# Performance work log

Measured on AMD Instinct MI355X. Metric: run time of the kernel, lower is better.

Reference implementation:

```python
import jax, jax.numpy as jnp
import numpy as np

MARGIN = 1.0
EPS = 1e-6  # torch F.pairwise_distance default eps, added elementwise to (x - y)
NEG_INF = -1e30
POS_INF = 1e30


def _pairwise_dist_matrix(e):
    # D[i,j] = || e_i - e_j + EPS ||_2, expanded so we never materialize [B,B,D]:
    # ||d + eps||^2 = ||d||^2 + 2*eps*sum(d) + Dfeat*eps^2,  d = e_i - e_j
    sq = jnp.sum(e * e, axis=1)          # [B]
    s = jnp.sum(e, axis=1)               # [B]
    d2 = (sq[:, None] + sq[None, :] - 2.0 * (e @ e.T)
          + 2.0 * EPS * (s[:, None] - s[None, :])
          + e.shape[1] * (EPS * EPS))
    return jnp.sqrt(jnp.maximum(d2, 0.0))  # [B,B]


def _pdist(x, y):
    # F.pairwise_distance(p=2): ||x - y + eps||
    return jnp.sqrt(jnp.sum(jnp.square(x - y + EPS), axis=-1))


def setup_inputs() -> dict:
    B, D = 4096, 128
    key = jax.random.key(0)
    k1, k2, k3, k4 = jax.random.split(key, 4)
    embedding = jax.random.normal(k1, (B, D), dtype=jnp.float32)
    # label space == batch, each label appears exactly once in the batch
    target_idx = jax.random.permutation(k2, B).astype(jnp.int32)
    positive_idxs = jax.random.bernoulli(k3, 0.02, (B, B))  # [B, L] label-space mask
    negative_idxs = jax.random.bernoulli(k4, 0.5, (B, B))
    return {"embedding": embedding, "target_idx": target_idx,
            "positive_idxs": positive_idxs, "negative_idxs": negative_idxs}


def reference(embedding, target_idx, positive_idxs, negative_idxs):
    # Mining happens under no_grad in the original module.
    dm = jax.lax.stop_gradient(_pairwise_dist_matrix(embedding))  # [B,B]
    # batch j is a positive/negative candidate for anchor i iff its label is flagged
    pos_mask = positive_idxs[:, target_idx]  # [B,B] bool
    neg_mask = negative_idxs[:, target_idx]
    pos_idx = jnp.argmax(jnp.where(pos_mask, dm, NEG_INF), axis=1)  # hardest positive
    neg_idx = jnp.argmin(jnp.where(neg_mask, dm, POS_INF), axis=1)  # hardest negative
    valid = jnp.any(pos_mask, axis=1) & jnp.any(neg_mask, axis=1)
    a = embedding
    p = embedding[pos_idx]
    n = embedding[neg_idx]
    ap = _pdist(a, p)
    an = _pdist(a, n)
    pn = _pdist(p, n)
    loss = jax.nn.relu(ap - jnp.minimum(an, pn) + MARGIN)
    w = valid.astype(loss.dtype)
    return jnp.sum(loss * w) / jnp.maximum(jnp.sum(w), 1.0)
```

## Files before the change

kernel.cpp:

```cpp
#include <hip/hip_runtime.h>
#include <stdint.h>

#define BN 4096
#define DD 128
#define EPSF 1e-6f
#define MARGINF 1.0f

typedef unsigned long long ull;
typedef unsigned short ushort;
typedef short short8 __attribute__((ext_vector_type(8)));
typedef float f32x4 __attribute__((ext_vector_type(4)));

__device__ __forceinline__ unsigned int ord_f32(float f) {
    unsigned int u = __float_as_uint(f);
    return (u & 0x80000000u) ? ~u : (u | 0x80000000u);
}
__device__ __forceinline__ ushort bf16_rne(float x) {
    unsigned int u = __float_as_uint(x);
    return (ushort)((u + 0x7FFFu + ((u >> 16) & 1u)) >> 16);
}
__device__ __forceinline__ unsigned int pack8(ull v) {
    v &= 0x0F0F0F0F0F0F0F0FULL;
    v = (v | (v >> 4)) & 0x00FF00FF00FF00FFULL;
    v = (v | (v >> 8)) & 0x0000FFFF0000FFFFULL;
    v = (v | (v >> 16));
    return (unsigned int)v;
}

__global__ void k_prep(const float* __restrict__ e, const int* __restrict__ tidx,
                       float* __restrict__ sq, float* __restrict__ s,
                       int* __restrict__ inv, ull* __restrict__ pk, ull* __restrict__ nk,
                       unsigned int* __restrict__ ehi) {
    int w = threadIdx.x >> 6, lane = threadIdx.x & 63;
    int row = blockIdx.x * 4 + w;
    float2 v = ((const float2*)(e + (size_t)row * DD))[lane];
    ushort hx = bf16_rne(v.x), hy = bf16_rne(v.y);
    ehi[row * 64 + lane] = (unsigned int)hx | ((unsigned int)hy << 16);
    float ss = v.x + v.y;
    float qq = v.x * v.x + v.y * v.y;
    #pragma unroll
    for (int off = 32; off > 0; off >>= 1) {
        ss += __shfl_down(ss, off);
        qq += __shfl_down(qq, off);
    }
    if (lane == 0) {
        sq[row] = qq; s[row] = ss;
        inv[tidx[row]] = row;
        pk[row] = 0ULL; nk[row] = 0ULL;
    }
}

__global__ __launch_bounds__(256, 4)
void k_select(const ushort* __restrict__ ehi,
              const int* __restrict__ pos, const int* __restrict__ neg,
              const float* __restrict__ sq, const float* __restrict__ s,
              const int* __restrict__ inv,
              ull* __restrict__ pkey, ull* __restrict__ nkey) {
    __shared__ __align__(16) char smem[36864];
    __shared__ float rjl[128];
    __shared__ int jvs[128];

    const int tid = threadIdx.x;
    const int lane = tid & 63;
    const int w = tid >> 6, wr = w >> 1, wc = w & 1;
    const int lrow = lane & 15, quad = lane >> 4;
    const int i0 = blockIdx.x * 128, c0 = blockIdx.y * 128;

    if (tid < 128) {
        int j = inv[c0 + tid];
        jvs[tid] = j;
        rjl[tid] = sq[j] - 2.0f * EPSF * s[j];
    }

    unsigned char* nibP = (unsigned char*)smem;
    unsigned char* nibN = (unsigned char*)(smem + 4096);
    {
        const int4* pbase = (const int4*)(pos + (size_t)i0 * BN + c0);
        const int4* nbase = (const int4*)(neg + (size_t)i0 * BN + c0);
        #pragma unroll
        for (int p = 0; p < 16; p++) {
            int flat = p * 256 + tid;
            int r = flat >> 5, q = flat & 31;
            size_t idx = (size_t)r * (BN / 4) + q;
            int4 P = pbase[idx];
            int4 N = nbase[idx];
            unsigned int pm = (unsigned int)(P.x != 0) | ((unsigned int)(P.y != 0) << 1)
                            | ((unsigned int)(P.z != 0) << 2) | ((unsigned int)(P.w != 0) << 3);
            unsigned int nm = (unsigned int)(N.x != 0) | ((unsigned int)(N.y != 0) << 1)
                            | ((unsigned int)(N.z != 0) << 2) | ((unsigned int)(N.w != 0) << 3);
            nibP[r * 32 + q] = (unsigned char)pm;
            nibN[r * 32 + q] = (unsigned char)nm;
        }
    }
    __syncthreads();

    ull pw, nw;
    {
        int off = (tid >> 1) * 32 + (tid & 1) * 16;
        ull lo = *(const ull*)(nibP + off);
        ull hi = *(const ull*)(nibP + off + 8);
        pw = (ull)pack8(lo) | ((ull)pack8(hi) << 32);
        lo = *(const ull*)(nibN + off);
        hi = *(const ull*)(nibN + off + 8);
        nw = (ull)pack8(lo) | ((ull)pack8(hi) << 32);
    }
    __syncthreads();

    ushort* Bst = (ushort*)smem;
    #pragma unroll
    for (int it = 0; it < 8; it++) {
        int slot = it * 256 + tid;
        int r = slot >> 4, seg16 = slot & 15;
        int kc = seg16 >> 3, seg = seg16 & 7;
        int jr = jvs[r];
        int4 v = ((const int4*)ehi)[(size_t)jr * 16 + seg16];
        *(int4*)(Bst + (kc * 128 + r) * 72 + seg * 8) = v;
    }
    __syncthreads();

    f32x4 acc[4][4];
    #pragma unroll
    for (int rt = 0; rt < 4; rt++)
        #pragma unroll
        for (int ct = 0; ct < 4; ct++)
            acc[rt][ct] = (f32x4){0.f, 0.f, 0.f, 0.f};

    size_t abase[4];
    #pragma unroll
    for (int rt = 0; rt < 4; rt++)
        abase[rt] = (size_t)(i0 + wr * 64 + rt * 16 + lrow) * DD + quad * 8;

    #pragma unroll
    for (int ks = 0; ks < 4; ks++) {
        const int kc = ks >> 1, ksl = ks & 1;
        short8 ah[4];
        #pragma unroll
        for (int rt = 0; rt < 4; rt++)
            ah[rt] = *(const short8*)(ehi + abase[rt] + ks * 32);
        #pragma unroll
        for (int ct = 0; ct < 4; ct++) {
            const int bo = (kc * 128 + wc * 64 + ct * 16 + lrow) * 72 + ksl * 32 + quad * 8;
            short8 bh = *(const short8*)(Bst + bo);
            #pragma unroll
            for (int rt = 0; rt < 4; rt++)
                acc[rt][ct] = __builtin_amdgcn_mfma_f32_16x16x32_bf16(ah[rt], bh, acc[rt][ct], 0, 0, 0);
        }
    }

    __syncthreads();
    ull* pbl = (ull*)smem;
    ull* nbl = (ull*)(smem + 2048);
    pbl[tid] = pw;
    nbl[tid] = nw;
    __syncthreads();

    int jcol[4]; float rjc[4];
    #pragma unroll
    for (int ct = 0; ct < 4; ct++) {
        jcol[ct] = jvs[wc * 64 + ct * 16 + lrow];
        rjc[ct] = rjl[wc * 64 + ct * 16 + lrow];
    }
    ull* scrp = (ull*)(smem + 4096);
    ull* scrn = (ull*)(smem + 20480);
    #pragma unroll
    for (int rt = 0; rt < 4; rt++)
        #pragma unroll
        for (int t = 0; t < 4; t++) {
            const int row = wr * 64 + rt * 16 + quad * 4 + t;
            ull pb = pbl[row * 2 + wc] >> lrow;
            ull nb = nbl[row * 2 + wc] >> lrow;
            float bpv = -3.4e38f, bnv = 3.4e38f;
            int bpi = 0x7FFFFFFF, bni = 0x7FFFFFFF;
            #pragma unroll
            for (int ct = 0; ct < 4; ct++) {
                float m = rjc[ct] - 2.0f * acc[rt][ct][t];
                int j = jcol[ct];
                if ((pb >> (ct * 16)) & 1ULL) {
                    if (m > bpv || (m == bpv && j < bpi)) { bpv = m; bpi = j; }
                }
                if ((nb >> (ct * 16)) & 1ULL) {
                    if (m < bnv || (m == bnv && j < bni)) { bnv = m; bni = j; }
                }
            }
            ull kp = (bpi == 0x7FFFFFFF) ? 0ULL
                   : (((ull)ord_f32(bpv) << 32) | (ull)(0xFFFFFFFFu - (unsigned)bpi));
            ull kn = (bni == 0x7FFFFFFF) ? 0ULL
                   : (((ull)(~ord_f32(bnv)) << 32) | (ull)(0xFFFFFFFFu - (unsigned)bni));
            ull op = __shfl_xor(kp, 8); if (op > kp) kp = op;
            ull on = __shfl_xor(kn, 8); if (on > kn) kn = on;
            if (lrow < 8) {
                scrp[(wc * 8 + lrow) * 128 + row] = kp;
                scrn[(wc * 8 + lrow) * 128 + row] = kn;
            }
        }
    __syncthreads();
    if (tid < 128) {
        ull kp = 0ULL, kn = 0ULL;
        #pragma unroll
        for (int k = 0; k < 16; k++) {
            ull v = scrp[k * 128 + tid]; if (v > kp) kp = v;
            v = scrn[k * 128 + tid];     if (v > kn) kn = v;
        }
        if (kp) atomicMax(&pkey[i0 + tid], kp);
        if (kn) atomicMax(&nkey[i0 + tid], kn);
    }
}

__global__ void k_loss(const float* __restrict__ e,
                       const ull* __restrict__ pkey, const ull* __restrict__ nkey,
                       float* __restrict__ partials) {
    int w = threadIdx.x >> 6, lane = threadIdx.x & 63;
    int row = blockIdx.x * 4 + w;
    ull pk = pkey[row], nk = nkey[row];
    float loss = 0.0f, wt = 0.0f;
    if (pk != 0ULL && nk != 0ULL) {
        int pi = (int)(0xFFFFFFFFu - (unsigned)(pk & 0xFFFFFFFFu));
        int ni = (int)(0xFFFFFFFFu - (unsigned)(nk & 0xFFFFFFFFu));
        float2 av = ((const float2*)(e + (size_t)row * DD))[lane];
        float2 pv = ((const float2*)(e + (size_t)pi * DD))[lane];
        float2 nv = ((const float2*)(e + (size_t)ni * DD))[lane];
        float dx, dy;
        dx = av.x - pv.x + EPSF; dy = av.y - pv.y + EPSF;
        float ap2 = dx * dx + dy * dy;
        dx = av.x - nv.x + EPSF; dy = av.y - nv.y + EPSF;
        float an2 = dx * dx + dy * dy;
        dx = pv.x - nv.x + EPSF; dy = pv.y - nv.y + EPSF;
        float pn2 = dx * dx + dy * dy;
        #pragma unroll
        for (int off = 32; off > 0; off >>= 1) {
            ap2 += __shfl_down(ap2, off);
            an2 += __shfl_down(an2, off);
            pn2 += __shfl_down(pn2, off);
        }
        if (lane == 0) {
            float ap = sqrtf(ap2), an = sqrtf(an2), pn = sqrtf(pn2);
            loss = fmaxf(ap - fminf(an, pn) + MARGINF, 0.0f);
            wt = 1.0f;
        }
    }
    __shared__ float sl[4], sw[4];
    if (lane == 0) { sl[w] = loss; sw[w] = wt; }
    __syncthreads();
    if (threadIdx.x == 0) {
        partials[blockIdx.x * 2 + 0] = sl[0] + sl[1] + sl[2] + sl[3];
        partials[blockIdx.x * 2 + 1] = sw[0] + sw[1] + sw[2] + sw[3];
    }
}

__global__ void k_final(const float* __restrict__ partials, float* __restrict__ out) {
    int tid = threadIdx.x;
    float L = 0.0f, W = 0.0f;
    for (int i = 0; i < 4; i++) {
        int idx = tid + i * 256;
        L += partials[idx * 2];
        W += partials[idx * 2 + 1];
    }
    #pragma unroll
    for (int off = 32; off > 0; off >>= 1) {
        L += __shfl_down(L, off);
        W += __shfl_down(W, off);
    }
    __shared__ float sl[4], sw[4];
    int w = tid >> 6, lane = tid & 63;
    if (lane == 0) { sl[w] = L; sw[w] = W; }
    __syncthreads();
    if (tid == 0) {
        float Lt = sl[0] + sl[1] + sl[2] + sl[3];
        float Wt = sw[0] + sw[1] + sw[2] + sw[3];
        out[0] = Lt / fmaxf(Wt, 1.0f);
    }
}

extern "C" void kernel_launch(void* const* d_in, const int* in_sizes, int n_in,
                              void* d_out, int out_size, void* d_ws, size_t ws_size,
                              hipStream_t stream) {
    const float* e    = (const float*)d_in[0];
    const int*   tidx = (const int*)d_in[1];
    const int*   pos  = (const int*)d_in[2];
    const int*   neg  = (const int*)d_in[3];
    float* out = (float*)d_out;

    ull* pkey  = (ull*)d_ws;
    ull* nkey  = pkey + BN;
    float* sq  = (float*)(nkey + BN);
    float* s   = sq + BN;
    int* inv   = (int*)(s + BN);
    float* partials = (float*)(inv + BN);
    unsigned int* ehi = (unsigned int*)(partials + 2048);

    k_prep<<<BN / 4, 256, 0, stream>>>(e, tidx, sq, s, inv, pkey, nkey, ehi);
    dim3 grid(BN / 128, BN / 128);
    k_select<<<grid, 256, 0, stream>>>((const ushort*)ehi, pos, neg,
                                       sq, s, inv, pkey, nkey);
    k_loss<<<BN / 4, 256, 0, stream>>>(e, pkey, nkey, partials);
    k_final<<<1, 256, 0, stream>>>(partials, out);
}
```

Before: 185.9 us.

## Read masks directly in epilogue, pad scratch, fuse final reduction into loss kernel

The mask tiles are no longer staged in shared memory as nibble bitmasks. Each lane now reads its pos/neg int32 mask elements straight from global memory in the MFMA epilogue, and the argmax/argmin is simplified to a single combined-key max. The scratch reduction layout is padded (stride 17) to avoid LDS bank conflicts, and the final-sum kernel is merged into k_loss with a last-block-done atomic counter, which saves one launch. The epilogue mask loads are strided (16 lanes contiguous per row), so coalescing is worse than the old int4 bulk loads and the kernel may stall on the MFMA tail.

```diff
diff --git a/kernel.cpp b/kernel.cpp
--- a/kernel.cpp
+++ b/kernel.cpp
@@ -19,20 +19,14 @@
     unsigned int u = __float_as_uint(x);
     return (ushort)((u + 0x7FFFu + ((u >> 16) & 1u)) >> 16);
 }
-__device__ __forceinline__ unsigned int pack8(ull v) {
-    v &= 0x0F0F0F0F0F0F0F0FULL;
-    v = (v | (v >> 4)) & 0x00FF00FF00FF00FFULL;
-    v = (v | (v >> 8)) & 0x0000FFFF0000FFFFULL;
-    v = (v | (v >> 16));
-    return (unsigned int)v;
-}
 
 __global__ void k_prep(const float* __restrict__ e, const int* __restrict__ tidx,
                        float* __restrict__ sq, float* __restrict__ s,
                        int* __restrict__ inv, ull* __restrict__ pk, ull* __restrict__ nk,
-                       unsigned int* __restrict__ ehi) {
+                       unsigned int* __restrict__ ehi, unsigned int* __restrict__ cnt) {
     int w = threadIdx.x >> 6, lane = threadIdx.x & 63;
     int row = blockIdx.x * 4 + w;
+    if (blockIdx.x == 0 && threadIdx.x == 0) cnt[0] = 0u;
     float2 v = ((const float2*)(e + (size_t)row * DD))[lane];
     ushort hx = bf16_rne(v.x), hy = bf16_rne(v.y);
     ehi[row * 64 + lane] = (unsigned int)hx | ((unsigned int)hy << 16);
@@ -71,39 +65,6 @@
         jvs[tid] = j;
         rjl[tid] = sq[j] - 2.0f * EPSF * s[j];
     }
-
-    unsigned char* nibP = (unsigned char*)smem;
-    unsigned char* nibN = (unsigned char*)(smem + 4096);
-    {
-        const int4* pbase = (const int4*)(pos + (size_t)i0 * BN + c0);
-        const int4* nbase = (const int4*)(neg + (size_t)i0 * BN + c0);
-        #pragma unroll
-        for (int p = 0; p < 16; p++) {
-            int flat = p * 256 + tid;
-            int r = flat >> 5, q = flat & 31;
-            size_t idx = (size_t)r * (BN / 4) + q;
-            int4 P = pbase[idx];
-            int4 N = nbase[idx];
-            unsigned int pm = (unsigned int)(P.x != 0) | ((unsigned int)(P.y != 0) << 1)
-                            | ((unsigned int)(P.z != 0) << 2) | ((unsigned int)(P.w != 0) << 3);
-            unsigned int nm = (unsigned int)(N.x != 0) | ((unsigned int)(N.y != 0) << 1)
-                            | ((unsigned int)(N.z != 0) << 2) | ((unsigned int)(N.w != 0) << 3);
-            nibP[r * 32 + q] = (unsigned char)pm;
-            nibN[r * 32 + q] = (unsigned char)nm;
-        }
-    }
-    __syncthreads();
-
-    ull pw, nw;
-    {
-        int off = (tid >> 1) * 32 + (tid & 1) * 16;
-        ull lo = *(const ull*)(nibP + off);
-        ull hi = *(const ull*)(nibP + off + 8);
-        pw = (ull)pack8(lo) | ((ull)pack8(hi) << 32);
-        lo = *(const ull*)(nibN + off);
-        hi = *(const ull*)(nibN + off + 8);
-        nw = (ull)pack8(lo) | ((ull)pack8(hi) << 32);
-    }
     __syncthreads();
 
     ushort* Bst = (ushort*)smem;
@@ -148,58 +109,58 @@
     }
 
     __syncthreads();
-    ull* pbl = (ull*)smem;
-    ull* nbl = (ull*)(smem + 2048);
-    pbl[tid] = pw;
-    nbl[tid] = nw;
-    __syncthreads();
-
-    int jcol[4]; float rjc[4];
+
+    ull* scrp = (ull*)smem;
+    ull* scrn = (ull*)(smem + 17408);
+
+    unsigned int jninv[4]; float rjc[4];
     #pragma unroll
     for (int ct = 0; ct < 4; ct++) {
-        jcol[ct] = jvs[wc * 64 + ct * 16 + lrow];
-        rjc[ct] = rjl[wc * 64 + ct * 16 + lrow];
-    }
-    ull* scrp = (ull*)(smem + 4096);
-    ull* scrn = (ull*)(smem + 20480);
-    #pragma unroll
-    for (int rt = 0; rt < 4; rt++)
+        int cc = wc * 64 + ct * 16 + lrow;
+        jninv[ct] = 0xFFFFFFFFu - (unsigned int)jvs[cc];
+        rjc[ct] = rjl[cc];
+    }
+
+    const size_t mrow0 = (size_t)(i0 + wr * 64 + quad * 4) * BN + (size_t)(c0 + wc * 64 + lrow);
+    const int rbase = wr * 64 + quad * 4;
+
+    #pragma unroll
+    for (int rt = 0; rt < 4; rt++) {
         #pragma unroll
         for (int t = 0; t < 4; t++) {
-            const int row = wr * 64 + rt * 16 + quad * 4 + t;
-            ull pb = pbl[row * 2 + wc] >> lrow;
-            ull nb = nbl[row * 2 + wc] >> lrow;
-            float bpv = -3.4e38f, bnv = 3.4e38f;
-            int bpi = 0x7FFFFFFF, bni = 0x7FFFFFFF;
+            const size_t mb = mrow0 + (size_t)(rt * 16 + t) * BN;
+            int pd[4], nd[4];
+            #pragma unroll
+            for (int ct = 0; ct < 4; ct++) {
+                pd[ct] = pos[mb + ct * 16];
+                nd[ct] = neg[mb + ct * 16];
+            }
+            ull kp = 0ULL, kn = 0ULL;
             #pragma unroll
             for (int ct = 0; ct < 4; ct++) {
                 float m = rjc[ct] - 2.0f * acc[rt][ct][t];
-                int j = jcol[ct];
-                if ((pb >> (ct * 16)) & 1ULL) {
-                    if (m > bpv || (m == bpv && j < bpi)) { bpv = m; bpi = j; }
-                }
-                if ((nb >> (ct * 16)) & 1ULL) {
-                    if (m < bnv || (m == bnv && j < bni)) { bnv = m; bni = j; }
-                }
+                unsigned int om = ord_f32(m);
+                ull keyp = ((ull)om << 32) | (ull)jninv[ct];
+                ull keyn = ((ull)(om ^ 0xFFFFFFFFu) << 32) | (ull)jninv[ct];
+                if (pd[ct] != 0 && keyp > kp) kp = keyp;
+                if (nd[ct] != 0 && keyn > kn) kn = keyn;
             }
-            ull kp = (bpi == 0x7FFFFFFF) ? 0ULL
-                   : (((ull)ord_f32(bpv) << 32) | (ull)(0xFFFFFFFFu - (unsigned)bpi));
-            ull kn = (bni == 0x7FFFFFFF) ? 0ULL
-                   : (((ull)(~ord_f32(bnv)) << 32) | (ull)(0xFFFFFFFFu - (unsigned)bni));
             ull op = __shfl_xor(kp, 8); if (op > kp) kp = op;
             ull on = __shfl_xor(kn, 8); if (on > kn) kn = on;
             if (lrow < 8) {
-                scrp[(wc * 8 + lrow) * 128 + row] = kp;
-                scrn[(wc * 8 + lrow) * 128 + row] = kn;
+                const int row = rbase + rt * 16 + t;
+                scrp[row * 17 + wc * 8 + lrow] = kp;
+                scrn[row * 17 + wc * 8 + lrow] = kn;
             }
         }
+    }
     __syncthreads();
     if (tid < 128) {
         ull kp = 0ULL, kn = 0ULL;
         #pragma unroll
         for (int k = 0; k < 16; k++) {
-            ull v = scrp[k * 128 + tid]; if (v > kp) kp = v;
-            v = scrn[k * 128 + tid];     if (v > kn) kn = v;
+            ull v = scrp[tid * 17 + k]; if (v > kp) kp = v;
+            v = scrn[tid * 17 + k];     if (v > kn) kn = v;
         }
         if (kp) atomicMax(&pkey[i0 + tid], kp);
         if (kn) atomicMax(&nkey[i0 + tid], kn);
@@ -208,7 +169,8 @@
 
 __global__ void k_loss(const float* __restrict__ e,
                        const ull* __restrict__ pkey, const ull* __restrict__ nkey,
-                       float* __restrict__ partials) {
+                       float* __restrict__ partials, unsigned int* __restrict__ cnt,
+                       float* __restrict__ out) {
     int w = threadIdx.x >> 6, lane = threadIdx.x & 63;
     int row = blockIdx.x * 4 + w;
     ull pk = pkey[row], nk = nkey[row];
@@ -239,35 +201,42 @@
         }
     }
     __shared__ float sl[4], sw[4];
+    __shared__ unsigned int rank;
     if (lane == 0) { sl[w] = loss; sw[w] = wt; }
     __syncthreads();
     if (threadIdx.x == 0) {
-        partials[blockIdx.x * 2 + 0] = sl[0] + sl[1] + sl[2] + sl[3];
-        partials[blockIdx.x * 2 + 1] = sw[0] + sw[1] + sw[2] + sw[3];
-    }
-}
-
-__global__ void k_final(const float* __restrict__ partials, float* __restrict__ out) {
-    int tid = threadIdx.x;
-    float L = 0.0f, W = 0.0f;
-    for (int i = 0; i < 4; i++) {
-        int idx = tid + i * 256;
-        L += partials[idx * 2];
-        W += partials[idx * 2 + 1];
-    }
-    #pragma unroll
-    for (int off = 32; off > 0; off >>= 1) {
-        L += __shfl_down(L, off);
-        W += __shfl_down(W, off);
-    }
-    __shared__ float sl[4], sw[4];
-    int w = tid >> 6, lane = tid & 63;
-    if (lane == 0) { sl[w] = L; sw[w] = W; }
-    __syncthreads();
-    if (tid == 0) {
-        float Lt = sl[0] + sl[1] + sl[2] + sl[3];
-        float Wt = sw[0] + sw[1] + sw[2] + sw[3];
-        out[0] = Lt / fmaxf(Wt, 1.0f);
+        float L = sl[0] + sl[1] + sl[2] + sl[3];
+        float W = sw[0] + sw[1] + sw[2] + sw[3];
+        __hip_atomic_store(&partials[blockIdx.x * 2 + 0], L, __ATOMIC_RELAXED, __HIP_MEMORY_SCOPE_AGENT);
+        __hip_atomic_store(&partials[blockIdx.x * 2 + 1], W, __ATOMIC_RELAXED, __HIP_MEMORY_SCOPE_AGENT);
+        __threadfence();
+        rank = atomicAdd(cnt, 1u);
+    }
+    __syncthreads();
+    if (rank == (unsigned)(gridDim.x - 1)) {
+        __threadfence();
+        int tid = threadIdx.x;
+        float L = 0.0f, W = 0.0f;
+        #pragma unroll
+        for (int i = 0; i < 4; i++) {
+            int idx = tid + i * 256;
+            L += __hip_atomic_load(&partials[idx * 2 + 0], __ATOMIC_RELAXED, __HIP_MEMORY_SCOPE_AGENT);
+            W += __hip_atomic_load(&partials[idx * 2 + 1], __ATOMIC_RELAXED, __HIP_MEMORY_SCOPE_AGENT);
+        }
+        #pragma unroll
+        for (int off = 32; off > 0; off >>= 1) {
+            L += __shfl_down(L, off);
+            W += __shfl_down(W, off);
+        }
+        __shared__ float fl[4], fw[4];
+        int w2 = tid >> 6, l2 = tid & 63;
+        if (l2 == 0) { fl[w2] = L; fw[w2] = W; }
+        __syncthreads();
+        if (tid == 0) {
+            float Lt = fl[0] + fl[1] + fl[2] + fl[3];
+            float Wt = fw[0] + fw[1] + fw[2] + fw[3];
+            out[0] = Lt / fmaxf(Wt, 1.0f);
+        }
     }
 }
 
@@ -287,11 +256,11 @@
     int* inv   = (int*)(s + BN);
     float* partials = (float*)(inv + BN);
     unsigned int* ehi = (unsigned int*)(partials + 2048);
-
-    k_prep<<<BN / 4, 256, 0, stream>>>(e, tidx, sq, s, inv, pkey, nkey, ehi);
+    unsigned int* cnt = ehi + (size_t)BN * 64;
+
+    k_prep<<<BN / 4, 256, 0, stream>>>(e, tidx, sq, s, inv, pkey, nkey, ehi, cnt);
     dim3 grid(BN / 128, BN / 128);
     k_select<<<grid, 256, 0, stream>>>((const ushort*)ehi, pos, neg,
                                        sq, s, inv, pkey, nkey);
-    k_loss<<<BN / 4, 256, 0, stream>>>(e, pkey, nkey, partials);
-    k_final<<<1, 256, 0, stream>>>(partials, out);
-}
+    k_loss<<<BN / 4, 256, 0, stream>>>(e, pkey, nkey, partials, cnt, out);
+}
```

New measurement: 194.1 us. +4.5%, slower.
